# Kernel optimization log

Hardware: AMD Instinct MI355X
Metric: run time of the kernel (lower is better)

Reference implementation:

```python
import jax, jax.numpy as jnp
import numpy as np

Na, Nb, G, D = 200000, 300000, 10000, 256
EPS_GATE = 1e-6
EPS_BN = 1e-5


def setup_inputs() -> dict:
    key = jax.random.key(0)
    ks = jax.random.split(key, 10)
    h = jax.random.normal(ks[0], (Na, D), jnp.float32)
    e = jax.random.normal(ks[1], (Nb, D), jnp.float32)
    u = jax.random.normal(ks[2], (G, D), jnp.float32)
    snorm_n = jax.random.uniform(ks[3], (Na, 1), jnp.float32)
    snorm_e = jax.random.uniform(ks[4], (Nb, 1), jnp.float32)
    # 9 linear layers A..I stacked: W[i] is [out,in] like nn.Linear.weight
    W = jax.random.normal(ks[5], (9, D, D), jnp.float32) / np.sqrt(D)
    b = jax.random.normal(ks[6], (9, D), jnp.float32) * 0.01
    bn_gamma = jnp.ones((3, D), jnp.float32)
    bn_beta = jnp.zeros((3, D), jnp.float32)
    bond_atoms = jax.random.randint(ks[7], (Nb, 2), 0, Na, dtype=jnp.int32)
    atom2graph = jax.random.randint(ks[8], (Na,), 0, G, dtype=jnp.int32)
    bond2graph = jax.random.randint(ks[9], (Nb,), 0, G, dtype=jnp.int32)
    return {"h": h, "e": e, "u": u, "snorm_n": snorm_n, "snorm_e": snorm_e,
            "W": W, "b": b, "bn_gamma": bn_gamma, "bn_beta": bn_beta,
            "bond_atoms": bond_atoms, "atom2graph": atom2graph,
            "bond2graph": bond2graph}


def reference(h, e, u, snorm_n, snorm_e, W, b, bn_gamma, bn_beta,
              bond_atoms, atom2graph, bond2graph):
    lin = lambda x, i: x @ W[i].T + b[i]
    seg = lambda d, ids, n: jax.ops.segment_sum(d, ids, num_segments=n)

    Ah, Be, Cu = lin(h, 0), lin(e, 1), lin(u, 2)
    Dh, Eh, Fu = lin(h, 3), lin(h, 4), lin(u, 5)
    Gh, He, Iu = lin(h, 6), lin(e, 7), lin(u, 8)

    i0, i1 = bond_atoms[:, 0], bond_atoms[:, 1]
    # bond update: sum of Ah over its 2 atoms + self-loop Be + graph's Cu
    e_new = Ah[i0] + Ah[i1] + Be + Cu[bond2graph]

    # gated b2a aggregation: each endpoint receives sigma(e)*Eh[other endpoint]
    sigma = jax.nn.sigmoid(e_new)  # [Nb, D]
    num = seg(sigma * Eh[i1], i0, Na) + seg(sigma * Eh[i0], i1, Na)
    den = seg(sigma, i0, Na) + seg(sigma, i1, Na)
    h_new = Dh + num / (den + EPS_GATE) + Fu[atom2graph]

    # global update: mean over atoms of Gh + mean over bonds of He + self Iu
    ones_a = jnp.ones((Na, 1), h.dtype)
    ones_b = jnp.ones((Nb, 1), e.dtype)
    cnt_a = jnp.maximum(seg(ones_a, atom2graph, G), 1.0)
    cnt_b = jnp.maximum(seg(ones_b, bond2graph, G), 1.0)
    u_new = seg(Gh, atom2graph, G) / cnt_a + seg(He, bond2graph, G) / cnt_b + Iu

    # graph norm (atoms and bonds only, as in the torch code)
    h_new = h_new * snorm_n
    e_new = e_new * snorm_e

    def bn(x, g, beta):
        m = x.mean(axis=0)
        v = x.var(axis=0)  # biased var, matching BN training normalization
        return g * (x - m) * jax.lax.rsqrt(v + EPS_BN) + beta

    h_out = jax.nn.elu(bn(h_new, bn_gamma[0], bn_beta[0]))
    e_out = jax.nn.elu(bn(e_new, bn_gamma[1], bn_beta[1]))
    u_out = jax.nn.elu(bn(u_new, bn_gamma[2], bn_beta[2]))
    # residual=False (default), dropout=0 -> identity
    return h_out, e_out, u_out
```

## Files before the change

kernel.cpp:

```cpp
#include <hip/hip_runtime.h>
#include <stdint.h>

#define NA 200000
#define NB 300000
#define NG 10000
#define DD 256
#define EPS_GATE 1e-6f
#define EPS_BN 1e-5f

typedef short bf16x8 __attribute__((ext_vector_type(8)));
typedef float f32x4 __attribute__((ext_vector_type(4)));

__device__ __forceinline__ unsigned short f2bf(float f){
  union { float f; uint32_t u; } v; v.f = f;
  uint32_t uu = v.u;
  uint32_t r = (uu + 0x7FFFu + ((uu >> 16) & 1u)) >> 16;
  return (unsigned short)r;
}
__device__ __forceinline__ float bf2f(unsigned short s){
  union { uint32_t u; float f; } v; v.u = ((uint32_t)s) << 16; return v.f;
}

__device__ __forceinline__ void gload_lds16(const unsigned short* g, unsigned short* l){
  __builtin_amdgcn_global_load_lds(
      (const __attribute__((address_space(1))) unsigned int*)g,
      (__attribute__((address_space(3))) unsigned int*)l, 16, 0, 0);
}

__global__ void k_zero(int4* p, size_t n16){
  for (size_t i = blockIdx.x*(size_t)blockDim.x + threadIdx.x; i < n16;
       i += (size_t)gridDim.x*blockDim.x)
    p[i] = make_int4(0,0,0,0);
}

__global__ void k_wconv(const float* __restrict__ W, unsigned short* __restrict__ Wbf, int n4){
  for (int i = blockIdx.x*blockDim.x + threadIdx.x; i < n4; i += gridDim.x*blockDim.x){
    float4 v = ((const float4*)W)[i];
    ushort4 o; o.x = f2bf(v.x); o.y = f2bf(v.y); o.z = f2bf(v.z); o.w = f2bf(v.w);
    ((ushort4*)Wbf)[i] = o;
  }
}

__global__ __launch_bounds__(512, 4) void k_gemm4(
    const float* __restrict__ x, int Nrows,
    const unsigned short* __restrict__ Wbf,
    const float* __restrict__ bias,
    unsigned short* __restrict__ Y,
    int j0, int j1, int j2, int j3, int nW)
{
  __shared__ unsigned short As[128*256];
  __shared__ unsigned short Bs[256*32];
  const int tid  = threadIdx.x;
  const int wave = tid >> 6, lane = tid & 63;
  const int l15  = lane & 15, kq = lane >> 4;
  const int wr   = wave >> 2, wc = wave & 3;
  const int rowBase = blockIdx.x * 128;

  #pragma unroll
  for (int i = 0; i < 8; ++i){
    int idx = i*512 + tid;
    int r = idx >> 5, g = idx & 31;
    f32x4 v0 = {0.f,0.f,0.f,0.f}, v1 = {0.f,0.f,0.f,0.f};
    if (rowBase + r < Nrows){
      const float* p = x + (size_t)(rowBase + r)*DD + g*8;
      v0 = *(const f32x4*)p; v1 = *(const f32x4*)(p + 4);
    }
    uint32_t d[4];
    const uint32_t* a  = (const uint32_t*)&v0;
    const uint32_t* b2 = (const uint32_t*)&v1;
    d[0] = __builtin_amdgcn_perm(a[1],  a[0],  0x07060302u);
    d[1] = __builtin_amdgcn_perm(a[3],  a[2],  0x07060302u);
    d[2] = __builtin_amdgcn_perm(b2[1], b2[0], 0x07060302u);
    d[3] = __builtin_amdgcn_perm(b2[3], b2[2], 0x07060302u);
    int gs = g ^ ((r & 15) << 1);
    *(int4*)(As + r*256 + gs*8) = *(int4*)d;
  }

  const int sB = kq ^ ((l15 >> 1) & 3);

  for (int jj = 0; jj < nW; ++jj){
    const int j = (jj==0) ? j0 : (jj==1) ? j1 : (jj==2) ? j2 : j3;
    const unsigned short* Wj = Wbf + (size_t)j*DD*DD;
    const float* bj = bias + (size_t)j*DD;
    unsigned short* Yj = Y + (size_t)jj*Nrows*DD;

    f32x4 acc[4][4];
    #pragma unroll
    for (int m=0;m<4;m++)
      #pragma unroll
      for (int n=0;n<4;n++)
        acc[m][n] = (f32x4){0.f,0.f,0.f,0.f};

    for (int ks = 0; ks < 8; ++ks){
      __syncthreads();
      #pragma unroll
      for (int i = 0; i < 2; ++i){
        int idx  = i*512 + tid;
        int row  = idx >> 2;
        int slot = idx & 3;
        int srcg = slot ^ ((row >> 1) & 3);
        gload_lds16(Wj + (size_t)row*DD + ks*32 + srcg*8,
                    Bs + ((size_t)i*512 + wave*64)*8);
      }
      __syncthreads();

      bf16x8 afr[4], bfr[4];
      #pragma unroll
      for (int m=0;m<4;m++){
        int row = wr*64 + 16*m + l15;
        int gs = (ks*4 + kq) ^ (l15 << 1);
        afr[m] = *(const bf16x8*)(As + row*256 + gs*8);
      }
      #pragma unroll
      for (int n=0;n<4;n++){
        int row = wc*64 + 16*n + l15;
        bfr[n] = *(const bf16x8*)(Bs + row*32 + sB*8);
      }
      #pragma unroll
      for (int m=0;m<4;m++)
        #pragma unroll
        for (int n=0;n<4;n++)
          acc[m][n] = __builtin_amdgcn_mfma_f32_16x16x32_bf16(afr[m], bfr[n], acc[m][n], 0,0,0);
    }

    #pragma unroll
    for (int m=0;m<4;m++){
      int row0 = rowBase + wr*64 + 16*m + 4*kq;
      #pragma unroll
      for (int n=0;n<4;n++){
        int col = wc*64 + 16*n + l15;
        float bv = bj[col];
        #pragma unroll
        for (int r=0;r<4;r++){
          int row = row0 + r;
          if (row < Nrows) Yj[(size_t)row*DD + col] = f2bf(acc[m][n][r] + bv);
        }
      }
    }
  }
}

__global__ void k_hist(const int* __restrict__ ba, const int* __restrict__ b2g,
                       const int* __restrict__ a2g,
                       int* deg, int* cntb, int* cnta){
  int stride = gridDim.x*blockDim.x;
  for (int i = blockIdx.x*blockDim.x + threadIdx.x; i < NB; i += stride){
    atomicAdd(&deg[ba[2*i]],   1);
    atomicAdd(&deg[ba[2*i+1]], 1);
    atomicAdd(&cntb[b2g[i]],   1);
  }
  for (int i = blockIdx.x*blockDim.x + threadIdx.x; i < NA; i += stride)
    atomicAdd(&cnta[a2g[i]], 1);
}

__global__ void k_scan_partials(const int* __restrict__ in, int n, int* __restrict__ part){
  __shared__ int sd[256];
  int base = blockIdx.x*2048;
  int s = 0;
  #pragma unroll
  for (int i=0;i<8;i++){
    int idx = base + threadIdx.x*8 + i;
    if (idx < n) s += in[idx];
  }
  sd[threadIdx.x] = s;
  __syncthreads();
  for (int off=128; off>0; off>>=1){
    if (threadIdx.x < off) sd[threadIdx.x] += sd[threadIdx.x+off];
    __syncthreads();
  }
  if (threadIdx.x==0) part[blockIdx.x] = sd[0];
}
__global__ void k_scan_small(int* part, int nb){
  if (threadIdx.x==0 && blockIdx.x==0){
    int run = 0;
    for (int i=0;i<nb;i++){ int v = part[i]; part[i] = run; run += v; }
    part[nb] = run;
  }
}
__global__ void k_scan_final(const int* __restrict__ in, int n,
                             const int* __restrict__ part, int* __restrict__ outp){
  __shared__ int sd[256];
  int base = blockIdx.x*2048;
  int loc[8];
  int s = 0;
  #pragma unroll
  for (int i=0;i<8;i++){
    int idx = base + threadIdx.x*8 + i;
    int v = (idx < n) ? in[idx] : 0;
    loc[i] = s; s += v;
  }
  sd[threadIdx.x] = s;
  __syncthreads();
  int mine = s;
  for (int off=1; off<256; off<<=1){
    int add = (threadIdx.x >= off) ? sd[threadIdx.x - off] : 0;
    __syncthreads();
    sd[threadIdx.x] += add;
    __syncthreads();
  }
  int b0 = part[blockIdx.x] + sd[threadIdx.x] - mine;
  #pragma unroll
  for (int i=0;i<8;i++){
    int idx = base + threadIdx.x*8 + i;
    if (idx < n) outp[idx] = b0 + loc[i];
  }
  if (blockIdx.x==0 && threadIdx.x==0) outp[n] = part[gridDim.x];
}

__global__ void k_scatter_atoms(const int* __restrict__ a2g, const int* __restrict__ goffa,
                                int* cura, int* alist){
  for (int i = blockIdx.x*blockDim.x + threadIdx.x; i < NA; i += gridDim.x*blockDim.x){
    int g = a2g[i];
    int p = atomicAdd(&cura[g], 1);
    alist[goffa[g] + p] = i;
  }
}
__global__ void k_scatter_bonds(const int* __restrict__ ba, const int* __restrict__ b2g,
                                const int* __restrict__ goffb, int* curb, int* blist,
                                const int* __restrict__ aoff, int* cur_atom,
                                int* incb, int* inco){
  for (int i = blockIdx.x*blockDim.x + threadIdx.x; i < NB; i += gridDim.x*blockDim.x){
    int g = b2g[i];
    int p = atomicAdd(&curb[g], 1);
    blist[goffb[g] + p] = i;
    int i0 = ba[2*i], i1 = ba[2*i+1];
    int q0 = atomicAdd(&cur_atom[i0], 1);
    incb[aoff[i0]+q0] = i; inco[aoff[i0]+q0] = i1;
    int q1 = atomicAdd(&cur_atom[i1], 1);
    incb[aoff[i1]+q1] = i; inco[aoff[i1]+q1] = i0;
  }
}

__global__ __launch_bounds__(256) void k_bond(
    const unsigned short* __restrict__ Ah, const unsigned short* __restrict__ Be,
    const unsigned short* __restrict__ Cu,
    const int* __restrict__ ba, const int* __restrict__ b2g,
    const float* __restrict__ sne,
    unsigned short* __restrict__ Sg, float* __restrict__ e_pre,
    float* esum, float* esumsq)
{
  const int wave = threadIdx.x >> 6, lane = threadIdx.x & 63;
  float s1[4] = {0,0,0,0}, s2[4] = {0,0,0,0};
  const int wstride = gridDim.x*4;
  for (int bond = blockIdx.x*4 + wave; bond < NB; bond += wstride){
    int i0 = ba[2*bond], i1 = ba[2*bond+1];
    int g  = b2g[bond];
    float sn = sne[bond];
    ushort4 a0 = *(const ushort4*)(Ah + (size_t)i0*DD + lane*4);
    ushort4 a1 = *(const ushort4*)(Ah + (size_t)i1*DD + lane*4);
    ushort4 be = *(const ushort4*)(Be + (size_t)bond*DD + lane*4);
    ushort4 cu = *(const ushort4*)(Cu + (size_t)g*DD + lane*4);
    float e0 = bf2f(a0.x)+bf2f(a1.x)+bf2f(be.x)+bf2f(cu.x);
    float e1 = bf2f(a0.y)+bf2f(a1.y)+bf2f(be.y)+bf2f(cu.y);
    float e2 = bf2f(a0.z)+bf2f(a1.z)+bf2f(be.z)+bf2f(cu.z);
    float e3 = bf2f(a0.w)+bf2f(a1.w)+bf2f(be.w)+bf2f(cu.w);
    ushort4 sg;
    sg.x = f2bf(1.f/(1.f+__expf(-e0)));
    sg.y = f2bf(1.f/(1.f+__expf(-e1)));
    sg.z = f2bf(1.f/(1.f+__expf(-e2)));
    sg.w = f2bf(1.f/(1.f+__expf(-e3)));
    *(ushort4*)(Sg + (size_t)bond*DD + lane*4) = sg;
    float4 ep; ep.x = e0*sn; ep.y = e1*sn; ep.z = e2*sn; ep.w = e3*sn;
    *(float4*)(e_pre + (size_t)bond*DD + lane*4) = ep;
    s1[0]+=ep.x; s2[0]+=ep.x*ep.x;
    s1[1]+=ep.y; s2[1]+=ep.y*ep.y;
    s1[2]+=ep.z; s2[2]+=ep.z*ep.z;
    s1[3]+=ep.w; s2[3]+=ep.w*ep.w;
  }
  __shared__ float red[4*DD];
  #pragma unroll
  for (int c=0;c<4;c++) red[wave*DD + lane*4 + c] = s1[c];
  __syncthreads();
  if (threadIdx.x < DD){
    float t = red[threadIdx.x] + red[DD+threadIdx.x] + red[2*DD+threadIdx.x] + red[3*DD+threadIdx.x];
    atomicAdd(&esum[threadIdx.x], t);
  }
  __syncthreads();
  #pragma unroll
  for (int c=0;c<4;c++) red[wave*DD + lane*4 + c] = s2[c];
  __syncthreads();
  if (threadIdx.x < DD){
    float t = red[threadIdx.x] + red[DD+threadIdx.x] + red[2*DD+threadIdx.x] + red[3*DD+threadIdx.x];
    atomicAdd(&esumsq[threadIdx.x], t);
  }
}

__global__ __launch_bounds__(256) void k_atom(
    const unsigned short* __restrict__ Dh, const unsigned short* __restrict__ Eh,
    const unsigned short* __restrict__ Fu, const unsigned short* __restrict__ Sg,
    const int* __restrict__ aoff, const int* __restrict__ incb, const int* __restrict__ inco,
    const int* __restrict__ a2g, const float* __restrict__ snn,
    float* __restrict__ h_pre, float* hsum, float* hsumsq)
{
  const int wave = threadIdx.x >> 6, lane = threadIdx.x & 63;
  float s1[4] = {0,0,0,0}, s2[4] = {0,0,0,0};
  const int wstride = gridDim.x*4;
  for (int a = blockIdx.x*4 + wave; a < NA; a += wstride){
    int j0 = aoff[a], j1 = aoff[a+1];
    float num[4] = {0,0,0,0}, den[4] = {0,0,0,0};
    for (int j = j0; j < j1; ++j){
      int bond = incb[j], other = inco[j];
      ushort4 sg = *(const ushort4*)(Sg + (size_t)bond*DD + lane*4);
      ushort4 eo = *(const ushort4*)(Eh + (size_t)other*DD + lane*4);
      float g0 = bf2f(sg.x), g1 = bf2f(sg.y), g2 = bf2f(sg.z), g3 = bf2f(sg.w);
      num[0] += g0*bf2f(eo.x); num[1] += g1*bf2f(eo.y);
      num[2] += g2*bf2f(eo.z); num[3] += g3*bf2f(eo.w);
      den[0] += g0; den[1] += g1; den[2] += g2; den[3] += g3;
    }
    int g = a2g[a]; float sn = snn[a];
    ushort4 dh = *(const ushort4*)(Dh + (size_t)a*DD + lane*4);
    ushort4 fu = *(const ushort4*)(Fu + (size_t)g*DD + lane*4);
    float4 hv;
    hv.x = (bf2f(dh.x) + num[0]/(den[0]+EPS_GATE) + bf2f(fu.x))*sn;
    hv.y = (bf2f(dh.y) + num[1]/(den[1]+EPS_GATE) + bf2f(fu.y))*sn;
    hv.z = (bf2f(dh.z) + num[2]/(den[2]+EPS_GATE) + bf2f(fu.z))*sn;
    hv.w = (bf2f(dh.w) + num[3]/(den[3]+EPS_GATE) + bf2f(fu.w))*sn;
    *(float4*)(h_pre + (size_t)a*DD + lane*4) = hv;
    s1[0]+=hv.x; s2[0]+=hv.x*hv.x;
    s1[1]+=hv.y; s2[1]+=hv.y*hv.y;
    s1[2]+=hv.z; s2[2]+=hv.z*hv.z;
    s1[3]+=hv.w; s2[3]+=hv.w*hv.w;
  }
  __shared__ float red[4*DD];
  #pragma unroll
  for (int c=0;c<4;c++) red[wave*DD + lane*4 + c] = s1[c];
  __syncthreads();
  if (threadIdx.x < DD){
    float t = red[threadIdx.x] + red[DD+threadIdx.x] + red[2*DD+threadIdx.x] + red[3*DD+threadIdx.x];
    atomicAdd(&hsum[threadIdx.x], t);
  }
  __syncthreads();
  #pragma unroll
  for (int c=0;c<4;c++) red[wave*DD + lane*4 + c] = s2[c];
  __syncthreads();
  if (threadIdx.x < DD){
    float t = red[threadIdx.x] + red[DD+threadIdx.x] + red[2*DD+threadIdx.x] + red[3*DD+threadIdx.x];
    atomicAdd(&hsumsq[threadIdx.x], t);
  }
}

__global__ __launch_bounds__(256) void k_graph(
    const unsigned short* __restrict__ Gh, const unsigned short* __restrict__ He,
    const unsigned short* __restrict__ Iu,
    const int* __restrict__ goffa, const int* __restrict__ alist,
    const int* __restrict__ goffb, const int* __restrict__ blist,
    float* __restrict__ u_pre)
{
  int g = blockIdx.x, t = threadIdx.x;
  int a0 = goffa[g], a1 = goffa[g+1];
  float sA = 0.f;
  for (int i = a0; i < a1; ++i) sA += bf2f(Gh[(size_t)alist[i]*DD + t]);
  int b0 = goffb[g], b1 = goffb[g+1];
  float sB = 0.f;
  for (int i = b0; i < b1; ++i) sB += bf2f(He[(size_t)blist[i]*DD + t]);
  float cA = (float)max(a1 - a0, 1);
  float cB = (float)max(b1 - b0, 1);
  u_pre[(size_t)g*DD + t] = sA/cA + sB/cB + bf2f(Iu[(size_t)g*DD + t]);
}

__global__ void k_ustats(const float* __restrict__ u_pre, float* usum, float* usumsq){
  int t = threadIdx.x;
  float s = 0.f, s2 = 0.f;
  for (int g = blockIdx.x; g < NG; g += gridDim.x){
    float v = u_pre[(size_t)g*DD + t];
    s += v; s2 += v*v;
  }
  atomicAdd(&usum[t], s);
  atomicAdd(&usumsq[t], s2);
}

__global__ void k_bnfin(const float* __restrict__ sums, const float* __restrict__ sumsq,
                        float* __restrict__ mr){
  int o = blockIdx.x, t = threadIdx.x;
  float n = (o==0) ? (float)NA : (o==1) ? (float)NB : (float)NG;
  float m = sums[o*DD+t]/n;
  float v = sumsq[o*DD+t]/n - m*m;
  mr[o*2*DD + t]      = m;
  mr[o*2*DD + DD + t] = rsqrtf(fmaxf(v, 0.f) + EPS_BN);
}

__global__ __launch_bounds__(256) void k_norm(
    float* __restrict__ buf, size_t nrows,
    const float* __restrict__ mr, const float* __restrict__ gamma,
    const float* __restrict__ beta)
{
  __shared__ float sm[DD], sr[DD], sg[DD], sb[DD];
  int t = threadIdx.x;
  sm[t] = mr[t]; sr[t] = mr[DD+t]; sg[t] = gamma[t]; sb[t] = beta[t];
  __syncthreads();
  size_t total = nrows*(DD/4);
  for (size_t i = blockIdx.x*(size_t)blockDim.x + t; i < total;
       i += (size_t)gridDim.x*blockDim.x){
    int c = ((int)(i & 63))*4;
    float4 v = ((float4*)buf)[i];
    float z0 = (v.x - sm[c+0])*sr[c+0]*sg[c+0] + sb[c+0];
    float z1 = (v.y - sm[c+1])*sr[c+1]*sg[c+1] + sb[c+1];
    float z2 = (v.z - sm[c+2])*sr[c+2]*sg[c+2] + sb[c+2];
    float z3 = (v.w - sm[c+3])*sr[c+3]*sg[c+3] + sb[c+3];
    v.x = z0 > 0.f ? z0 : expm1f(z0);
    v.y = z1 > 0.f ? z1 : expm1f(z1);
    v.z = z2 > 0.f ? z2 : expm1f(z2);
    v.w = z3 > 0.f ? z3 : expm1f(z3);
    ((float4*)buf)[i] = v;
  }
}

extern "C" void kernel_launch(void* const* d_in, const int* in_sizes, int n_in,
                              void* d_out, int out_size, void* d_ws, size_t ws_size,
                              hipStream_t stream)
{
  (void)in_sizes; (void)n_in; (void)out_size;
  const float* h   = (const float*)d_in[0];
  const float* e   = (const float*)d_in[1];
  const float* u   = (const float*)d_in[2];
  const float* snn = (const float*)d_in[3];
  const float* sne = (const float*)d_in[4];
  const float* W   = (const float*)d_in[5];
  const float* b   = (const float*)d_in[6];
  const float* gamma = (const float*)d_in[7];
  const float* beta  = (const float*)d_in[8];
  const int* ba  = (const int*)d_in[9];
  const int* a2g = (const int*)d_in[10];
  const int* b2g = (const int*)d_in[11];

  float* outp  = (float*)d_out;
  float* h_pre = outp;
  float* e_pre = outp + (size_t)NA*DD;
  float* u_pre = outp + (size_t)(NA+NB)*DD;

  char* ws = (char*)d_ws;
  size_t off = 0;
  auto alloc = [&](size_t bytes)->char* {
    char* p = ws + off;
    off += (bytes + 255) & ~(size_t)255;
    return p;
  };
  unsigned short* Wbf = (unsigned short*)alloc((size_t)9*DD*DD*2);
  unsigned short* Yh  = (unsigned short*)alloc((size_t)4*NA*DD*2);
  unsigned short* Ye  = (unsigned short*)alloc((size_t)2*NB*DD*2);
  unsigned short* Yu  = (unsigned short*)alloc((size_t)3*NG*DD*2);
  unsigned short* Sg  = (unsigned short*)alloc((size_t)NB*DD*2);
  int* aoff  = (int*)alloc((size_t)(NA+1)*4);
  int* goffa = (int*)alloc((size_t)(NG+1)*4);
  int* goffb = (int*)alloc((size_t)(NG+1)*4);
  int* alist = (int*)alloc((size_t)NA*4);
  int* blist = (int*)alloc((size_t)NB*4);
  int* incb  = (int*)alloc((size_t)2*NB*4);
  int* inco  = (int*)alloc((size_t)2*NB*4);
  int* part  = (int*)alloc(1024);
  float* mr  = (float*)alloc((size_t)3*2*DD*4);
  char* zz   = ws + off;
  int* deg      = (int*)alloc((size_t)NA*4);
  int* cur_atom = (int*)alloc((size_t)NA*4);
  int* cnta  = (int*)alloc((size_t)NG*4);
  int* cntb  = (int*)alloc((size_t)NG*4);
  int* cura  = (int*)alloc((size_t)NG*4);
  int* curb  = (int*)alloc((size_t)NG*4);
  float* sums  = (float*)alloc((size_t)3*DD*4);
  float* sumsq = (float*)alloc((size_t)3*DD*4);
  size_t zbytes = (size_t)((ws + off) - zz);

  if (ws_size < off) return;

  unsigned short* Ah = Yh;
  unsigned short* Dh = Yh + (size_t)1*NA*DD;
  unsigned short* Eh = Yh + (size_t)2*NA*DD;
  unsigned short* Gh = Yh + (size_t)3*NA*DD;
  unsigned short* Be = Ye;
  unsigned short* He = Ye + (size_t)NB*DD;
  unsigned short* Cu = Yu;
  unsigned short* Fu = Yu + (size_t)1*NG*DD;
  unsigned short* Iu = Yu + (size_t)2*NG*DD;

  k_zero<<<256, 256, 0, stream>>>((int4*)zz, zbytes/16);
  k_wconv<<<288, 256, 0, stream>>>(W, Wbf, 9*DD*DD/4);

  k_gemm4<<<(NA+127)/128, 512, 0, stream>>>(h, NA, Wbf, b, Yh, 0,3,4,6, 4);
  k_gemm4<<<(NB+127)/128, 512, 0, stream>>>(e, NB, Wbf, b, Ye, 1,7,0,0, 2);
  k_gemm4<<<(NG+127)/128, 512, 0, stream>>>(u, NG, Wbf, b, Yu, 2,5,8,0, 3);

  k_hist<<<1024, 256, 0, stream>>>(ba, b2g, a2g, deg, cntb, cnta);

  k_scan_partials<<<98, 256, 0, stream>>>(deg, NA, part);
  k_scan_small<<<1, 64, 0, stream>>>(part, 98);
  k_scan_final<<<98, 256, 0, stream>>>(deg, NA, part, aoff);
  k_scan_partials<<<5, 256, 0, stream>>>(cnta, NG, part);
  k_scan_small<<<1, 64, 0, stream>>>(part, 5);
  k_scan_final<<<5, 256, 0, stream>>>(cnta, NG, part, goffa);
  k_scan_partials<<<5, 256, 0, stream>>>(cntb, NG, part);
  k_scan_small<<<1, 64, 0, stream>>>(part, 5);
  k_scan_final<<<5, 256, 0, stream>>>(cntb, NG, part, goffb);

  k_scatter_atoms<<<512, 256, 0, stream>>>(a2g, goffa, cura, alist);
  k_scatter_bonds<<<512, 256, 0, stream>>>(ba, b2g, goffb, curb, blist,
                                           aoff, cur_atom, incb, inco);

  k_bond<<<2048, 256, 0, stream>>>(Ah, Be, Cu, ba, b2g, sne, Sg, e_pre,
                                   sums + DD, sumsq + DD);
  k_atom<<<2048, 256, 0, stream>>>(Dh, Eh, Fu, Sg, aoff, incb, inco, a2g, snn,
                                   h_pre, sums + 0, sumsq + 0);
  k_graph<<<NG, 256, 0, stream>>>(Gh, He, Iu, goffa, alist, goffb, blist, u_pre);
  k_ustats<<<40, 256, 0, stream>>>(u_pre, sums + 2*DD, sumsq + 2*DD);

  k_bnfin<<<3, 256, 0, stream>>>(sums, sumsq, mr);

  k_norm<<<2048, 256, 0, stream>>>(h_pre, (size_t)NA, mr + 0,      gamma + 0,    beta + 0);
  k_norm<<<2048, 256, 0, stream>>>(e_pre, (size_t)NB, mr + 2*DD,   gamma + DD,   beta + DD);
  k_norm<<<64,   256, 0, stream>>>(u_pre, (size_t)NG, mr + 4*DD,   gamma + 2*DD, beta + 2*DD);
}
```

Before: 1.605 ms.

## Software-pipeline weight tile loads through registers in fused GEMM kernel

```diff
diff --git a/kernel.cpp b/kernel.cpp
--- a/kernel.cpp
+++ b/kernel.cpp
@@ -21,12 +21,6 @@
   union { uint32_t u; float f; } v; v.u = ((uint32_t)s) << 16; return v.f;
 }
 
-__device__ __forceinline__ void gload_lds16(const unsigned short* g, unsigned short* l){
-  __builtin_amdgcn_global_load_lds(
-      (const __attribute__((address_space(1))) unsigned int*)g,
-      (__attribute__((address_space(3))) unsigned int*)l, 16, 0, 0);
-}
-
 __global__ void k_zero(int4* p, size_t n16){
   for (size_t i = blockIdx.x*(size_t)blockDim.x + threadIdx.x; i < n16;
        i += (size_t)gridDim.x*blockDim.x)
@@ -41,7 +35,7 @@
   }
 }
 
-__global__ __launch_bounds__(512, 4) void k_gemm4(
+__global__ __launch_bounds__(512, 4) void k_gemm5(
     const float* __restrict__ x, int Nrows,
     const unsigned short* __restrict__ Wbf,
     const float* __restrict__ bias,
@@ -77,66 +71,100 @@
   }
 
   const int sB = kq ^ ((l15 >> 1) & 3);
-
-  for (int jj = 0; jj < nW; ++jj){
-    const int j = (jj==0) ? j0 : (jj==1) ? j1 : (jj==2) ? j2 : j3;
-    const unsigned short* Wj = Wbf + (size_t)j*DD*DD;
-    const float* bj = bias + (size_t)j*DD;
-    unsigned short* Yj = Y + (size_t)jj*Nrows*DD;
-
-    f32x4 acc[4][4];
+  const int IT = nW*8;
+
+  int4 breg0, breg1;
+  auto issueB = [&](int it){
+    int jj = it >> 3, ks = it & 7;
+    int j  = (jj==0) ? j0 : (jj==1) ? j1 : (jj==2) ? j2 : j3;
+    const unsigned short* Wj = Wbf + (size_t)j*DD*DD + ks*32;
+    {
+      int idx = tid;
+      int row = idx >> 2, slot = idx & 3;
+      int srcg = slot ^ ((row >> 1) & 3);
+      breg0 = *(const int4*)(Wj + (size_t)row*DD + srcg*8);
+    }
+    {
+      int idx = 512 + tid;
+      int row = idx >> 2, slot = idx & 3;
+      int srcg = slot ^ ((row >> 1) & 3);
+      breg1 = *(const int4*)(Wj + (size_t)row*DD + srcg*8);
+    }
+  };
+  auto writeB = [&](){
+    *(int4*)(Bs + (size_t)tid*8)         = breg0;
+    *(int4*)(Bs + (size_t)(512+tid)*8)   = breg1;
+  };
+
+  issueB(0);
+  __syncthreads();
+  writeB();
+  asm volatile("s_waitcnt lgkmcnt(0)" ::: "memory");
+  __builtin_amdgcn_s_barrier();
+  __builtin_amdgcn_sched_barrier(0);
+
+  f32x4 acc[4][4];
+  #pragma unroll
+  for (int m=0;m<4;m++)
+    #pragma unroll
+    for (int n=0;n<4;n++)
+      acc[m][n] = (f32x4){0.f,0.f,0.f,0.f};
+
+  for (int it = 0; it < IT; ++it){
+    const int jj = it >> 3, ks = it & 7;
+    if (it+1 < IT) issueB(it+1);
+
+    bf16x8 afr[4], bfr[4];
+    #pragma unroll
+    for (int m=0;m<4;m++){
+      int row = wr*64 + 16*m + l15;
+      int gs = (ks*4 + kq) ^ (l15 << 1);
+      afr[m] = *(const bf16x8*)(As + row*256 + gs*8);
+    }
+    #pragma unroll
+    for (int n=0;n<4;n++){
+      int row = wc*64 + 16*n + l15;
+      bfr[n] = *(const bf16x8*)(Bs + row*32 + sB*8);
+    }
     #pragma unroll
     for (int m=0;m<4;m++)
       #pragma unroll
       for (int n=0;n<4;n++)
-        acc[m][n] = (f32x4){0.f,0.f,0.f,0.f};
-
-    for (int ks = 0; ks < 8; ++ks){
-      __syncthreads();
-      #pragma unroll
-      for (int i = 0; i < 2; ++i){
-        int idx  = i*512 + tid;
-        int row  = idx >> 2;
-        int slot = idx & 3;
-        int srcg = slot ^ ((row >> 1) & 3);
-        gload_lds16(Wj + (size_t)row*DD + ks*32 + srcg*8,
-                    Bs + ((size_t)i*512 + wave*64)*8);
-      }
-      __syncthreads();
-
-      bf16x8 afr[4], bfr[4];
+        acc[m][n] = __builtin_amdgcn_mfma_f32_16x16x32_bf16(afr[m], bfr[n], acc[m][n], 0,0,0);
+
+    if (ks == 7){
+      const int j = (jj==0) ? j0 : (jj==1) ? j1 : (jj==2) ? j2 : j3;
+      const float* bj = bias + (size_t)j*DD;
+      unsigned short* Yj = Y + (size_t)jj*Nrows*DD;
       #pragma unroll
       for (int m=0;m<4;m++){
-        int row = wr*64 + 16*m + l15;
-        int gs = (ks*4 + kq) ^ (l15 << 1);
-        afr[m] = *(const bf16x8*)(As + row*256 + gs*8);
-      }
-      #pragma unroll
-      for (int n=0;n<4;n++){
-        int row = wc*64 + 16*n + l15;
-        bfr[n] = *(const bf16x8*)(Bs + row*32 + sB*8);
+        int row0 = rowBase + wr*64 + 16*m + 4*kq;
+        #pragma unroll
+        for (int n=0;n<4;n++){
+          int col = wc*64 + 16*n + l15;
+          float bv = bj[col];
+          #pragma unroll
+          for (int r=0;r<4;r++){
+            int row = row0 + r;
+            if (row < Nrows) Yj[(size_t)row*DD + col] = f2bf(acc[m][n][r] + bv);
+          }
+        }
       }
       #pragma unroll
       for (int m=0;m<4;m++)
         #pragma unroll
         for (int n=0;n<4;n++)
-          acc[m][n] = __builtin_amdgcn_mfma_f32_16x16x32_bf16(afr[m], bfr[n], acc[m][n], 0,0,0);
-    }
-
-    #pragma unroll
-    for (int m=0;m<4;m++){
-      int row0 = rowBase + wr*64 + 16*m + 4*kq;
-      #pragma unroll
-      for (int n=0;n<4;n++){
-        int col = wc*64 + 16*n + l15;
-        float bv = bj[col];
-        #pragma unroll
-        for (int r=0;r<4;r++){
-          int row = row0 + r;
-          if (row < Nrows) Yj[(size_t)row*DD + col] = f2bf(acc[m][n][r] + bv);
-        }
-      }
-    }
+          acc[m][n] = (f32x4){0.f,0.f,0.f,0.f};
+    }
+
+    __builtin_amdgcn_s_barrier();
+    __builtin_amdgcn_sched_barrier(0);
+    if (it+1 < IT){
+      writeB();
+      asm volatile("s_waitcnt lgkmcnt(0)" ::: "memory");
+    }
+    __builtin_amdgcn_s_barrier();
+    __builtin_amdgcn_sched_barrier(0);
   }
 }
 
@@ -475,9 +503,9 @@
   k_zero<<<256, 256, 0, stream>>>((int4*)zz, zbytes/16);
   k_wconv<<<288, 256, 0, stream>>>(W, Wbf, 9*DD*DD/4);
 
-  k_gemm4<<<(NA+127)/128, 512, 0, stream>>>(h, NA, Wbf, b, Yh, 0,3,4,6, 4);
-  k_gemm4<<<(NB+127)/128, 512, 0, stream>>>(e, NB, Wbf, b, Ye, 1,7,0,0, 2);
-  k_gemm4<<<(NG+127)/128, 512, 0, stream>>>(u, NG, Wbf, b, Yu, 2,5,8,0, 3);
+  k_gemm5<<<(NA+127)/128, 512, 0, stream>>>(h, NA, Wbf, b, Yh, 0,3,4,6, 4);
+  k_gemm5<<<(NB+127)/128, 512, 0, stream>>>(e, NB, Wbf, b, Ye, 1,7,0,0, 2);
+  k_gemm5<<<(NG+127)/128, 512, 0, stream>>>(u, NG, Wbf, b, Yu, 2,5,8,0, 3);
 
   k_hist<<<1024, 256, 0, stream>>>(ba, b2g, a2g, deg, cntb, cnta);
 
```

Measured after the change: 1.704 ms. 1.06x slower.

## Double-buffer weight tiles and shrink GEMM blocks to 64 rows

Applied to the files above, without the earlier changes.

```diff
diff --git a/kernel.cpp b/kernel.cpp
--- a/kernel.cpp
+++ b/kernel.cpp
@@ -41,24 +41,23 @@
   }
 }
 
-__global__ __launch_bounds__(512, 4) void k_gemm4(
+__global__ __launch_bounds__(256, 2) void k_gemm6(
     const float* __restrict__ x, int Nrows,
     const unsigned short* __restrict__ Wbf,
     const float* __restrict__ bias,
     unsigned short* __restrict__ Y,
     int j0, int j1, int j2, int j3, int nW)
 {
-  __shared__ unsigned short As[128*256];
-  __shared__ unsigned short Bs[256*32];
+  __shared__ unsigned short As[64*256];
+  __shared__ unsigned short Bs[2*256*32];
   const int tid  = threadIdx.x;
   const int wave = tid >> 6, lane = tid & 63;
   const int l15  = lane & 15, kq = lane >> 4;
-  const int wr   = wave >> 2, wc = wave & 3;
-  const int rowBase = blockIdx.x * 128;
+  const int rowBase = blockIdx.x * 64;
 
   #pragma unroll
   for (int i = 0; i < 8; ++i){
-    int idx = i*512 + tid;
+    int idx = i*256 + tid;
     int r = idx >> 5, g = idx & 31;
     f32x4 v0 = {0.f,0.f,0.f,0.f}, v1 = {0.f,0.f,0.f,0.f};
     if (rowBase + r < Nrows){
@@ -77,66 +76,85 @@
   }
 
   const int sB = kq ^ ((l15 >> 1) & 3);
-
-  for (int jj = 0; jj < nW; ++jj){
-    const int j = (jj==0) ? j0 : (jj==1) ? j1 : (jj==2) ? j2 : j3;
-    const unsigned short* Wj = Wbf + (size_t)j*DD*DD;
-    const float* bj = bias + (size_t)j*DD;
-    unsigned short* Yj = Y + (size_t)jj*Nrows*DD;
-
-    f32x4 acc[4][4];
+  const int IT = nW*8;
+
+  auto pick = [&](int jj)->int { return (jj==0) ? j0 : (jj==1) ? j1 : (jj==2) ? j2 : j3; };
+
+  auto stageB = [&](int it, int buf){
+    int jj = it >> 3, ks = it & 7;
+    const unsigned short* Wj = Wbf + (size_t)pick(jj)*DD*DD + ks*32;
+    unsigned short* dst = Bs + (size_t)buf*(256*32);
+    #pragma unroll
+    for (int i = 0; i < 4; ++i){
+      int idx  = i*256 + tid;
+      int row  = idx >> 2;
+      int slot = idx & 3;
+      int srcg = slot ^ ((row >> 1) & 3);
+      gload_lds16(Wj + (size_t)row*DD + srcg*8,
+                  dst + ((size_t)i*256 + wave*64)*8);
+    }
+  };
+
+  stageB(0, 0);
+  __syncthreads();
+  int cur = 0;
+
+  f32x4 acc[4][4];
+  #pragma unroll
+  for (int m=0;m<4;m++)
+    #pragma unroll
+    for (int n=0;n<4;n++)
+      acc[m][n] = (f32x4){0.f,0.f,0.f,0.f};
+
+  for (int it = 0; it < IT; ++it){
+    const int jj = it >> 3, ks = it & 7;
+    if (it+1 < IT) stageB(it+1, cur ^ 1);
+
+    const unsigned short* Bb = Bs + (size_t)cur*(256*32);
+    bf16x8 afr[4], bfr[4];
+    #pragma unroll
+    for (int m=0;m<4;m++){
+      int row = 16*m + l15;
+      int gs = (ks*4 + kq) ^ (l15 << 1);
+      afr[m] = *(const bf16x8*)(As + row*256 + gs*8);
+    }
+    #pragma unroll
+    for (int n=0;n<4;n++){
+      int row = wave*64 + 16*n + l15;
+      bfr[n] = *(const bf16x8*)(Bb + row*32 + sB*8);
+    }
     #pragma unroll
     for (int m=0;m<4;m++)
       #pragma unroll
       for (int n=0;n<4;n++)
-        acc[m][n] = (f32x4){0.f,0.f,0.f,0.f};
-
-    for (int ks = 0; ks < 8; ++ks){
-      __syncthreads();
-      #pragma unroll
-      for (int i = 0; i < 2; ++i){
-        int idx  = i*512 + tid;
-        int row  = idx >> 2;
-        int slot = idx & 3;
-        int srcg = slot ^ ((row >> 1) & 3);
-        gload_lds16(Wj + (size_t)row*DD + ks*32 + srcg*8,
-                    Bs + ((size_t)i*512 + wave*64)*8);
-      }
-      __syncthreads();
-
-      bf16x8 afr[4], bfr[4];
+        acc[m][n] = __builtin_amdgcn_mfma_f32_16x16x32_bf16(afr[m], bfr[n], acc[m][n], 0,0,0);
+
+    if (ks == 7){
+      const float* bj = bias + (size_t)pick(jj)*DD;
+      unsigned short* Yj = Y + (size_t)jj*Nrows*DD;
       #pragma unroll
       for (int m=0;m<4;m++){
-        int row = wr*64 + 16*m + l15;
-        int gs = (ks*4 + kq) ^ (l15 << 1);
-        afr[m] = *(const bf16x8*)(As + row*256 + gs*8);
-      }
-      #pragma unroll
-      for (int n=0;n<4;n++){
-        int row = wc*64 + 16*n + l15;
-        bfr[n] = *(const bf16x8*)(Bs + row*32 + sB*8);
+        int row0 = rowBase + 16*m + 4*kq;
+        #pragma unroll
+        for (int n=0;n<4;n++){
+          int col = wave*64 + 16*n + l15;
+          float bv = bj[col];
+          #pragma unroll
+          for (int r=0;r<4;r++){
+            int row = row0 + r;
+            if (row < Nrows) Yj[(size_t)row*DD + col] = f2bf(acc[m][n][r] + bv);
+          }
+        }
       }
       #pragma unroll
       for (int m=0;m<4;m++)
         #pragma unroll
         for (int n=0;n<4;n++)
-          acc[m][n] = __builtin_amdgcn_mfma_f32_16x16x32_bf16(afr[m], bfr[n], acc[m][n], 0,0,0);
+          acc[m][n] = (f32x4){0.f,0.f,0.f,0.f};
     }
 
-    #pragma unroll
-    for (int m=0;m<4;m++){
-      int row0 = rowBase + wr*64 + 16*m + 4*kq;
-      #pragma unroll
-      for (int n=0;n<4;n++){
-        int col = wc*64 + 16*n + l15;
-        float bv = bj[col];
-        #pragma unroll
-        for (int r=0;r<4;r++){
-          int row = row0 + r;
-          if (row < Nrows) Yj[(size_t)row*DD + col] = f2bf(acc[m][n][r] + bv);
-        }
-      }
-    }
+    __syncthreads();
+    cur ^= 1;
   }
 }
 
@@ -475,9 +493,9 @@
   k_zero<<<256, 256, 0, stream>>>((int4*)zz, zbytes/16);
   k_wconv<<<288, 256, 0, stream>>>(W, Wbf, 9*DD*DD/4);
 
-  k_gemm4<<<(NA+127)/128, 512, 0, stream>>>(h, NA, Wbf, b, Yh, 0,3,4,6, 4);
-  k_gemm4<<<(NB+127)/128, 512, 0, stream>>>(e, NB, Wbf, b, Ye, 1,7,0,0, 2);
-  k_gemm4<<<(NG+127)/128, 512, 0, stream>>>(u, NG, Wbf, b, Yu, 2,5,8,0, 3);
+  k_gemm6<<<(NA+63)/64, 256, 0, stream>>>(h, NA, Wbf, b, Yh, 0,3,4,6, 4);
+  k_gemm6<<<(NB+63)/64, 256, 0, stream>>>(e, NB, Wbf, b, Ye, 1,7,0,0, 2);
+  k_gemm6<<<(NG+63)/64, 256, 0, stream>>>(u, NG, Wbf, b, Yu, 2,5,8,0, 3);
 
   k_hist<<<1024, 256, 0, stream>>>(ba, b2g, a2g, deg, cntb, cnta);
 
```

After: 1.768 ms. 10.2% more time.

## Double-buffer weight tiles in fused GEMM and shrink row tile to 96

Applied to the files above, without the earlier changes.

```diff
diff --git a/kernel.cpp b/kernel.cpp
--- a/kernel.cpp
+++ b/kernel.cpp
@@ -41,23 +41,23 @@
   }
 }
 
-__global__ __launch_bounds__(512, 4) void k_gemm4(
+__global__ __launch_bounds__(512, 4) void k_gemm8(
     const float* __restrict__ x, int Nrows,
     const unsigned short* __restrict__ Wbf,
     const float* __restrict__ bias,
     unsigned short* __restrict__ Y,
     int j0, int j1, int j2, int j3, int nW)
 {
-  __shared__ unsigned short As[128*256];
-  __shared__ unsigned short Bs[256*32];
+  __shared__ unsigned short As[96*256];
+  __shared__ unsigned short Bs[2*256*32];
   const int tid  = threadIdx.x;
   const int wave = tid >> 6, lane = tid & 63;
   const int l15  = lane & 15, kq = lane >> 4;
   const int wr   = wave >> 2, wc = wave & 3;
-  const int rowBase = blockIdx.x * 128;
-
-  #pragma unroll
-  for (int i = 0; i < 8; ++i){
+  const int rowBase = blockIdx.x * 96;
+
+  #pragma unroll
+  for (int i = 0; i < 6; ++i){
     int idx = i*512 + tid;
     int r = idx >> 5, g = idx & 31;
     f32x4 v0 = {0.f,0.f,0.f,0.f}, v1 = {0.f,0.f,0.f,0.f};
@@ -78,54 +78,71 @@
 
   const int sB = kq ^ ((l15 >> 1) & 3);
 
+  auto pick = [&](int jj)->int { return (jj==0) ? j0 : (jj==1) ? j1 : (jj==2) ? j2 : j3; };
+
+  auto stageB = [&](int j, int ks, int buf){
+    const unsigned short* Wj = Wbf + (size_t)j*DD*DD + ks*32;
+    unsigned short* dst = Bs + (size_t)buf*(256*32);
+    #pragma unroll
+    for (int i = 0; i < 2; ++i){
+      int idx  = i*512 + tid;
+      int row  = idx >> 2;
+      int slot = idx & 3;
+      int srcg = slot ^ ((row >> 1) & 3);
+      gload_lds16(Wj + (size_t)row*DD + srcg*8,
+                  dst + ((size_t)i*512 + wave*64)*8);
+    }
+  };
+
+  stageB(pick(0), 0, 0);
+  __syncthreads();
+
   for (int jj = 0; jj < nW; ++jj){
-    const int j = (jj==0) ? j0 : (jj==1) ? j1 : (jj==2) ? j2 : j3;
-    const unsigned short* Wj = Wbf + (size_t)j*DD*DD;
-    const float* bj = bias + (size_t)j*DD;
-    unsigned short* Yj = Y + (size_t)jj*Nrows*DD;
-
-    f32x4 acc[4][4];
+    const int j = pick(jj);
+    f32x4 acc[3][4];
     #pragma unroll
-    for (int m=0;m<4;m++)
+    for (int m=0;m<3;m++)
       #pragma unroll
       for (int n=0;n<4;n++)
         acc[m][n] = (f32x4){0.f,0.f,0.f,0.f};
 
+    #pragma unroll
     for (int ks = 0; ks < 8; ++ks){
-      __syncthreads();
+      if (ks < 7){
+        stageB(j, ks+1, (ks+1)&1);
+        asm volatile("s_waitcnt vmcnt(2)" ::: "memory");
+      } else {
+        asm volatile("s_waitcnt vmcnt(0)" ::: "memory");
+      }
+      __builtin_amdgcn_s_barrier();
+
+      const unsigned short* Bb = Bs + (size_t)(ks&1)*(256*32);
+      bf16x8 afr[3], bfr[4];
       #pragma unroll
-      for (int i = 0; i < 2; ++i){
-        int idx  = i*512 + tid;
-        int row  = idx >> 2;
-        int slot = idx & 3;
-        int srcg = slot ^ ((row >> 1) & 3);
-        gload_lds16(Wj + (size_t)row*DD + ks*32 + srcg*8,
-                    Bs + ((size_t)i*512 + wave*64)*8);
-      }
-      __syncthreads();
-
-      bf16x8 afr[4], bfr[4];
-      #pragma unroll
-      for (int m=0;m<4;m++){
-        int row = wr*64 + 16*m + l15;
+      for (int m=0;m<3;m++){
+        int row = wr*48 + 16*m + l15;
         int gs = (ks*4 + kq) ^ (l15 << 1);
         afr[m] = *(const bf16x8*)(As + row*256 + gs*8);
       }
       #pragma unroll
       for (int n=0;n<4;n++){
         int row = wc*64 + 16*n + l15;
-        bfr[n] = *(const bf16x8*)(Bs + row*32 + sB*8);
+        bfr[n] = *(const bf16x8*)(Bb + row*32 + sB*8);
       }
       #pragma unroll
-      for (int m=0;m<4;m++)
+      for (int m=0;m<3;m++)
         #pragma unroll
         for (int n=0;n<4;n++)
           acc[m][n] = __builtin_amdgcn_mfma_f32_16x16x32_bf16(afr[m], bfr[n], acc[m][n], 0,0,0);
+
+      __builtin_amdgcn_s_barrier();
     }
 
+    const float* bj = bias + (size_t)j*DD;
+    unsigned short* Yj = Y + (size_t)jj*Nrows*DD;
     #pragma unroll
-    for (int m=0;m<4;m++){
-      int row0 = rowBase + wr*64 + 16*m + 4*kq;
+    for (int m=0;m<3;m++){
+      int row0 = rowBase + wr*48 + 16*m + 4*kq;
       #pragma unroll
       for (int n=0;n<4;n++){
         int col = wc*64 + 16*n + l15;
@@ -137,6 +154,8 @@
         }
       }
     }
+
+    if (jj+1 < nW) stageB(pick(jj+1), 0, 0);
   }
 }
 
@@ -475,9 +494,9 @@
   k_zero<<<256, 256, 0, stream>>>((int4*)zz, zbytes/16);
   k_wconv<<<288, 256, 0, stream>>>(W, Wbf, 9*DD*DD/4);
 
-  k_gemm4<<<(NA+127)/128, 512, 0, stream>>>(h, NA, Wbf, b, Yh, 0,3,4,6, 4);
-  k_gemm4<<<(NB+127)/128, 512, 0, stream>>>(e, NB, Wbf, b, Ye, 1,7,0,0, 2);
-  k_gemm4<<<(NG+127)/128, 512, 0, stream>>>(u, NG, Wbf, b, Yu, 2,5,8,0, 3);
+  k_gemm8<<<(NA+95)/96, 512, 0, stream>>>(h, NA, Wbf, b, Yh, 0,3,4,6, 4);
+  k_gemm8<<<(NB+95)/96, 512, 0, stream>>>(e, NB, Wbf, b, Ye, 1,7,0,0, 2);
+  k_gemm8<<<(NG+95)/96, 512, 0, stream>>>(u, NG, Wbf, b, Yu, 2,5,8,0, 3);
 
   k_hist<<<1024, 256, 0, stream>>>(ba, b2g, a2g, deg, cntb, cnta);
 
```

Measured after the change: 1.539 ms. 4.1% less time.
